# Kernel optimization log

Measured on AMD Instinct MI355X. Metric: run time of the kernel, lower is better.

## Reference

```python
import jax, jax.numpy as jnp
import numpy as np

B, C, H, W = 8, 128, 256, 256
NH, WS = 8, 16
EPS = 1e-6


def setup_inputs() -> dict:
    key = jax.random.key(0)
    k1, k2, k3, k4 = jax.random.split(key, 4)
    return {
        "x1": jax.random.normal(k1, (B, C, H, W), dtype=jnp.float32),
        "x2": jax.random.normal(k2, (B, C, H, W), dtype=jnp.float32),
        "Wq": jax.random.normal(k3, (C, C), dtype=jnp.float32) * 0.05,
        "Wkv": jax.random.normal(k4, (2 * C, C), dtype=jnp.float32) * 0.05,
    }


def _windows(t, b, h, d, hh, ww, ws):
    # [B, C, Hp, Wp] -> [(B hh ww), h, d, ws*ws]
    t = t.reshape(b, h, d, hh, ws, ww, ws)
    t = t.transpose(0, 3, 5, 1, 2, 4, 6)  # B,hh,ww,h,d,ws1,ws2
    return t.reshape(b * hh * ww, h, d, ws * ws)


def reference(x1, x2, Wq, Wkv) -> jnp.ndarray:
    b, c, hgt, wid = x1.shape
    ws, nh = WS, NH
    d = c // nh
    # H, W are multiples of ws so pad() is a no-op
    hh, ww = hgt // ws, wid // ws
    n = ws * ws

    # 1x1 convs (no bias) == pointwise channel matmuls
    q = jnp.einsum('bchw,oc->bohw', x1, Wq)
    kv = jnp.einsum('bchw,oc->bohw', x2, Wkv)
    k, v = kv[:, :c], kv[:, c:]

    qw = _windows(q, b, nh, d, hh, ww, ws)  # [bw, h, d, n]
    kw = _windows(k, b, nh, d, hh, ww, ws)
    vw = _windows(v, b, nh, d, hh, ww, ws)

    # L2 normalize over the channel (d) axis, matching torch.norm(dim=-2)
    kw = kw / jnp.linalg.norm(kw, axis=-2, keepdims=True)
    qw = qw / jnp.linalg.norm(qw, axis=-2, keepdims=True)
    qw = qw.transpose(0, 1, 3, 2)  # [bw, h, n, d]

    # Taylor softmax normalizer: 1 / (ws^2 + q . sum_n(k))
    tailor = 1.0 / (n + jnp.einsum('bhnc,bhc->bhn', qw, kw.sum(-1) + EPS))

    # linear attention: (q @ (k @ v^T))
    kv_acc = jnp.einsum('bhmn,bhcn->bhmc', kw, vw)         # [bw, h, d, d]
    attn = jnp.einsum('bhnm,bhmc->bhcn', qw, kv_acc)       # [bw, h, d, n]
    attn = attn + vw.sum(-1, keepdims=True)                # + sum_n v broadcast
    attn = attn * tailor[:, :, None, :]

    # scatter windows back: [(B hh ww), h, d, n] -> [B, C, H, W]
    out = attn.reshape(b, hh, ww, nh, d, ws, ws)
    out = out.transpose(0, 3, 4, 1, 5, 2, 6).reshape(b, c, hgt, wid)
    return out
```

## Files before the change

### kernel.cpp

```cpp
#include <hip/hip_runtime.h>
#include <cstdint>


typedef short V8AB __attribute__((ext_vector_type(8)));
typedef float V4F  __attribute__((ext_vector_type(4)));

#define IMG_W   256
#define HWSZ    65536
#define CCH     128
#define EPSF    1e-6f

__device__ __forceinline__ unsigned short f2bits(float f) {
    return __builtin_bit_cast(unsigned short, (__bf16)f);
}
__device__ __forceinline__ float bits2f(unsigned int h) {
    return __builtin_bit_cast(float, h << 16);
}

__device__ __forceinline__ V8AB load_wfrag(const float* __restrict__ wrow) {
    float4 w0 = *(const float4*)(wrow);
    float4 w1 = *(const float4*)(wrow + 4);
    V8AB r;
    r[0] = (short)f2bits(w0.x); r[1] = (short)f2bits(w0.y);
    r[2] = (short)f2bits(w0.z); r[3] = (short)f2bits(w0.w);
    r[4] = (short)f2bits(w1.x); r[5] = (short)f2bits(w1.y);
    r[6] = (short)f2bits(w1.z); r[7] = (short)f2bits(w1.w);
    return r;
}

__device__ __forceinline__ void stage_input(const float* __restrict__ src,
                                            short* xbuf, int tid, int pixbase) {
    #pragma unroll
    for (int it = 0; it < 8; ++it) {
        int p  = it * 256 + tid;
        int t0 = 2 * (p & 127);
        int cg = p >> 7;
        int c0 = cg * 8;
        const float* g = src + (size_t)c0 * HWSZ + pixbase + (t0 >> 4) * IMG_W + (t0 & 15);
        float2 f[8];
        #pragma unroll
        for (int j = 0; j < 8; ++j)
            f[j] = *(const float2*)(g + (size_t)j * HWSZ);
        V8AB va, vb;
        #pragma unroll
        for (int j = 0; j < 8; ++j) {
            va[j] = (short)f2bits(f[j].x);
            vb[j] = (short)f2bits(f[j].y);
        }
        int ca = ((t0 >> 4) << 8) + ((cg >> 2) << 6) + ((cg & 3) << 4) + (t0 & 15);
        *(V8AB*)(xbuf + (size_t)ca * 8)       = va;
        *(V8AB*)(xbuf + (size_t)(ca + 1) * 8) = vb;
    }
}

__global__ __launch_bounds__(256, 2)
void lwm_fused_kernel(const float* __restrict__ x1, const float* __restrict__ x2,
                      const float* __restrict__ Wq, const float* __restrict__ Wkv,
                      float* __restrict__ out) {
    __shared__ __align__(16) short xbuf[32768];

    const int tid  = threadIdx.x;
    const int lane = tid & 63;
    const int wv   = tid >> 6;
    const int l15  = lane & 15;
    const int quad = lane >> 4;
    const int zhi  = quad >> 1;

    const int blk = blockIdx.x;
    const int b   = blk >> 8;
    const int wy  = (blk >> 4) & 15;
    const int wx  = blk & 15;
    const int pixbase = wy * 16 * IMG_W + wx * 16;

    const float* x1b  = x1 + (size_t)b * CCH * HWSZ;
    const float* x2b  = x2 + (size_t)b * CCH * HWSZ;
    float*       outb = out + (size_t)b * CCH * HWSZ;

    stage_input(x1b, xbuf, tid, pixbase);
    __syncthreads();

    unsigned int qnp[2][16][2];
    #pragma unroll
    for (int hh = 0; hh < 2; ++hh) {
        const int head = wv + 4 * hh;
        V8AB bq[4];
        #pragma unroll
        for (int ks = 0; ks < 4; ++ks)
            bq[ks] = load_wfrag(Wq + (size_t)(head * 16 + l15) * CCH + ks * 32 + quad * 8);
        #pragma unroll
        for (int mt = 0; mt < 16; ++mt) {
            V4F acc = {0.f, 0.f, 0.f, 0.f};
            #pragma unroll
            for (int ks = 0; ks < 4; ++ks) {
                V8AB a = *(const V8AB*)(xbuf + (size_t)(mt * 256 + ks * 64 + lane) * 8);
                acc = __builtin_amdgcn_mfma_f32_16x16x32_bf16(a, bq[ks], acc, 0, 0, 0);
            }
            unsigned int p0 = 0, p1 = 0;
            #pragma unroll
            for (int r = 0; r < 4; ++r) {
                float s = acc[r] * acc[r];
                s += __shfl_xor(s, 1); s += __shfl_xor(s, 2);
                s += __shfl_xor(s, 4); s += __shfl_xor(s, 8);
                float qn = acc[r] * rsqrtf(s);
                unsigned int u = f2bits(qn);
                if      (r == 0) p0  = u;
                else if (r == 1) p0 |= u << 16;
                else if (r == 2) p1  = u;
                else             p1 |= u << 16;
            }
            qnp[hh][mt][0] = p0;
            qnp[hh][mt][1] = p1;
        }
    }
    __syncthreads();

    stage_input(x2b, xbuf, tid, pixbase);
    __syncthreads();

    #pragma unroll
    for (int hh = 0; hh < 2; ++hh) {
        const int head = wv + 4 * hh;
        V8AB bk[4], bv[4];
        #pragma unroll
        for (int ks = 0; ks < 4; ++ks) {
            bk[ks] = load_wfrag(Wkv + (size_t)(head * 16 + l15) * CCH + ks * 32 + quad * 8);
            bv[ks] = load_wfrag(Wkv + (size_t)(CCH + head * 16 + l15) * CCH + ks * 32 + quad * 8);
        }

        float ksum = 0.f, vsum = 0.f;
        V4F kvacc = {0.f, 0.f, 0.f, 0.f};

        #pragma unroll
        for (int s2 = 0; s2 < 8; ++s2) {
            V4F aK0 = {0,0,0,0}, aK1 = {0,0,0,0}, aV0 = {0,0,0,0}, aV1 = {0,0,0,0};
            #pragma unroll
            for (int ks = 0; ks < 4; ++ks) {
                V8AB a0 = *(const V8AB*)(xbuf + (size_t)((2*s2    ) * 256 + ks * 64 + lane) * 8);
                V8AB a1 = *(const V8AB*)(xbuf + (size_t)((2*s2 + 1) * 256 + ks * 64 + lane) * 8);
                aK0 = __builtin_amdgcn_mfma_f32_16x16x32_bf16(a0, bk[ks], aK0, 0, 0, 0);
                aV0 = __builtin_amdgcn_mfma_f32_16x16x32_bf16(a0, bv[ks], aV0, 0, 0, 0);
                aK1 = __builtin_amdgcn_mfma_f32_16x16x32_bf16(a1, bk[ks], aK1, 0, 0, 0);
                aV1 = __builtin_amdgcn_mfma_f32_16x16x32_bf16(a1, bv[ks], aV1, 0, 0, 0);
            }
            float kn0[4], kn1[4];
            #pragma unroll
            for (int r = 0; r < 4; ++r) {
                float s = aK0[r] * aK0[r];
                s += __shfl_xor(s, 1); s += __shfl_xor(s, 2);
                s += __shfl_xor(s, 4); s += __shfl_xor(s, 8);
                kn0[r] = aK0[r] * rsqrtf(s);
                float t = aK1[r] * aK1[r];
                t += __shfl_xor(t, 1); t += __shfl_xor(t, 2);
                t += __shfl_xor(t, 4); t += __shfl_xor(t, 8);
                kn1[r] = aK1[r] * rsqrtf(t);
                ksum += kn0[r] + kn1[r];
                vsum += aV0[r] + aV1[r];
            }
            V8AB ka, vb;
            #pragma unroll
            for (int j = 0; j < 8; ++j) {
                int src = l15 + ((((quad & 1) * 2) + (j >> 2)) << 4);
                float k0 = __shfl(kn0[j & 3], src);
                float k1 = __shfl(kn1[j & 3], src);
                float v0 = __shfl(aV0[j & 3], src);
                float v1 = __shfl(aV1[j & 3], src);
                ka[j] = (short)f2bits(zhi ? k1 : k0);
                vb[j] = (short)f2bits(zhi ? v1 : v0);
            }
            kvacc = __builtin_amdgcn_mfma_f32_16x16x32_bf16(ka, vb, kvacc, 0, 0, 0);
        }

        ksum += __shfl_xor(ksum, 16); ksum += __shfl_xor(ksum, 32);
        vsum += __shfl_xor(vsum, 16); vsum += __shfl_xor(vsum, 32);
        const float ksf = ksum + EPSF;

        V8AB kvb;
        #pragma unroll
        for (int j = 0; j < 8; ++j) {
            int src = l15 + ((((quad & 1) * 2) + (j >> 2)) << 4);
            float kv = __shfl(kvacc[j & 3], src);
            kvb[j] = zhi ? (short)0 : (short)f2bits(kv);
        }
        float ks8[8];
        #pragma unroll
        for (int j = 0; j < 8; ++j)
            ks8[j] = __shfl(ksf, (quad & 1) * 8 + j);

        #pragma unroll
        for (int mt = 0; mt < 16; ++mt) {
            unsigned int q0 = qnp[hh][mt][0], q1 = qnp[hh][mt][1];
            V8AB qa;
            float pd = 0.f;
            #pragma unroll
            for (int j = 0; j < 8; ++j) {
                int src = ((quad & 1) * 8 + j) + ((l15 >> 2) << 4);
                unsigned int u0 = __shfl(q0, src);
                unsigned int u1 = __shfl(q1, src);
                unsigned int us = (l15 & 2) ? u1 : u0;
                unsigned int hs = (l15 & 1) ? (us >> 16) : (us & 0xffffu);
                qa[j] = zhi ? (short)0 : (short)hs;
                pd += (zhi ? 0.f : bits2f(hs)) * ks8[j];
            }
            pd += __shfl_xor(pd, 16); pd += __shfl_xor(pd, 32);
            float ta = 1.0f / (256.0f + pd);

            V4F z = {0.f, 0.f, 0.f, 0.f};
            V4F dacc = __builtin_amdgcn_mfma_f32_16x16x32_bf16(qa, kvb, z, 0, 0, 0);

            #pragma unroll
            for (int r = 0; r < 4; ++r) {
                float tl = __shfl(ta, quad * 4 + r);
                float o  = (dacc[r] + vsum) * tl;
                int col  = quad * 4 + r;
                outb[(size_t)(head * 16 + l15) * HWSZ + pixbase + mt * IMG_W + col] = o;
            }
        }
    }
}

extern "C" void kernel_launch(void* const* d_in, const int* in_sizes, int n_in,
                              void* d_out, int out_size, void* d_ws, size_t ws_size,
                              hipStream_t stream) {
    const float* x1  = (const float*)d_in[0];
    const float* x2  = (const float*)d_in[1];
    const float* Wq  = (const float*)d_in[2];
    const float* Wkv = (const float*)d_in[3];
    float* out = (float*)d_out;
    lwm_fused_kernel<<<dim3(2048), dim3(256), 0, stream>>>(x1, x2, Wq, Wkv, out);
}
```

Measured before the change: 826.6 us.

## Use 512 threads with one head per wave, vectorize staging and output stores

Doubles the block to 8 waves so each wave handles a single head, removing the two-head loop and halving per-thread q register storage. Input staging now loads float4 per channel and writes four bf16 fragments, and output writes are merged into one float4 store per lane. This aims to raise parallelism and memory-access width, at the cost of higher register pressure under launch_bounds(512,4) and the 64KB LDS buffer limiting occupancy.

```diff
diff --git a/kernel.cpp b/kernel.cpp
--- a/kernel.cpp
+++ b/kernel.cpp
@@ -31,29 +31,33 @@
 __device__ __forceinline__ void stage_input(const float* __restrict__ src,
                                             short* xbuf, int tid, int pixbase) {
     #pragma unroll
-    for (int it = 0; it < 8; ++it) {
-        int p  = it * 256 + tid;
-        int t0 = 2 * (p & 127);
-        int cg = p >> 7;
+    for (int it = 0; it < 2; ++it) {
+        int p  = it * 512 + tid;
+        int t0 = 4 * (p & 63);
+        int cg = p >> 6;
         int c0 = cg * 8;
         const float* g = src + (size_t)c0 * HWSZ + pixbase + (t0 >> 4) * IMG_W + (t0 & 15);
-        float2 f[8];
+        float4 f[8];
         #pragma unroll
         for (int j = 0; j < 8; ++j)
-            f[j] = *(const float2*)(g + (size_t)j * HWSZ);
-        V8AB va, vb;
+            f[j] = *(const float4*)(g + (size_t)j * HWSZ);
+        int ca = ((t0 >> 4) << 8) + ((cg >> 2) << 6) + ((cg & 3) << 4) + (t0 & 15);
+        V8AB v0, v1, v2, v3;
         #pragma unroll
         for (int j = 0; j < 8; ++j) {
-            va[j] = (short)f2bits(f[j].x);
-            vb[j] = (short)f2bits(f[j].y);
-        }
-        int ca = ((t0 >> 4) << 8) + ((cg >> 2) << 6) + ((cg & 3) << 4) + (t0 & 15);
-        *(V8AB*)(xbuf + (size_t)ca * 8)       = va;
-        *(V8AB*)(xbuf + (size_t)(ca + 1) * 8) = vb;
+            v0[j] = (short)f2bits(f[j].x);
+            v1[j] = (short)f2bits(f[j].y);
+            v2[j] = (short)f2bits(f[j].z);
+            v3[j] = (short)f2bits(f[j].w);
+        }
+        *(V8AB*)(xbuf + (size_t)(ca    ) * 8) = v0;
+        *(V8AB*)(xbuf + (size_t)(ca + 1) * 8) = v1;
+        *(V8AB*)(xbuf + (size_t)(ca + 2) * 8) = v2;
+        *(V8AB*)(xbuf + (size_t)(ca + 3) * 8) = v3;
     }
 }
 
-__global__ __launch_bounds__(256, 2)
+__global__ __launch_bounds__(512, 4)
 void lwm_fused_kernel(const float* __restrict__ x1, const float* __restrict__ x2,
                       const float* __restrict__ Wq, const float* __restrict__ Wkv,
                       float* __restrict__ out) {
@@ -61,7 +65,7 @@
 
     const int tid  = threadIdx.x;
     const int lane = tid & 63;
-    const int wv   = tid >> 6;
+    const int head = tid >> 6;
     const int l15  = lane & 15;
     const int quad = lane >> 4;
     const int zhi  = quad >> 1;
@@ -79,10 +83,8 @@
     stage_input(x1b, xbuf, tid, pixbase);
     __syncthreads();
 
-    unsigned int qnp[2][16][2];
-    #pragma unroll
-    for (int hh = 0; hh < 2; ++hh) {
-        const int head = wv + 4 * hh;
+    unsigned int qnp[16][2];
+    {
         V8AB bq[4];
         #pragma unroll
         for (int ks = 0; ks < 4; ++ks)
@@ -108,8 +110,8 @@
                 else if (r == 2) p1  = u;
                 else             p1 |= u << 16;
             }
-            qnp[hh][mt][0] = p0;
-            qnp[hh][mt][1] = p1;
+            qnp[mt][0] = p0;
+            qnp[mt][1] = p1;
         }
     }
     __syncthreads();
@@ -117,9 +119,7 @@
     stage_input(x2b, xbuf, tid, pixbase);
     __syncthreads();
 
-    #pragma unroll
-    for (int hh = 0; hh < 2; ++hh) {
-        const int head = wv + 4 * hh;
+    {
         V8AB bk[4], bv[4];
         #pragma unroll
         for (int ks = 0; ks < 4; ++ks) {
@@ -188,7 +188,7 @@
 
         #pragma unroll
         for (int mt = 0; mt < 16; ++mt) {
-            unsigned int q0 = qnp[hh][mt][0], q1 = qnp[hh][mt][1];
+            unsigned int q0 = qnp[mt][0], q1 = qnp[mt][1];
             V8AB qa;
             float pd = 0.f;
             #pragma unroll
@@ -207,13 +207,18 @@
             V4F z = {0.f, 0.f, 0.f, 0.f};
             V4F dacc = __builtin_amdgcn_mfma_f32_16x16x32_bf16(qa, kvb, z, 0, 0, 0);
 
-            #pragma unroll
-            for (int r = 0; r < 4; ++r) {
-                float tl = __shfl(ta, quad * 4 + r);
-                float o  = (dacc[r] + vsum) * tl;
-                int col  = quad * 4 + r;
-                outb[(size_t)(head * 16 + l15) * HWSZ + pixbase + mt * IMG_W + col] = o;
-            }
+            float4 o4;
+            {
+                float tl0 = __shfl(ta, quad * 4 + 0);
+                float tl1 = __shfl(ta, quad * 4 + 1);
+                float tl2 = __shfl(ta, quad * 4 + 2);
+                float tl3 = __shfl(ta, quad * 4 + 3);
+                o4.x = (dacc[0] + vsum) * tl0;
+                o4.y = (dacc[1] + vsum) * tl1;
+                o4.z = (dacc[2] + vsum) * tl2;
+                o4.w = (dacc[3] + vsum) * tl3;
+            }
+            *(float4*)(outb + (size_t)(head * 16 + l15) * HWSZ + pixbase + mt * IMG_W + quad * 4) = o4;
         }
     }
 }
@@ -226,5 +231,5 @@
     const float* Wq  = (const float*)d_in[2];
     const float* Wkv = (const float*)d_in[3];
     float* out = (float*)d_out;
-    lwm_fused_kernel<<<dim3(2048), dim3(256), 0, stream>>>(x1, x2, Wq, Wkv, out);
-}
+    lwm_fused_kernel<<<dim3(2048), dim3(512), 0, stream>>>(x1, x2, Wq, Wkv, out);
+}
```

Result: slower. 885.9 us (+7.2%).
